# Kernel optimization log

Hardware: AMD Instinct MI355X
Metric: run time of the kernel (lower is better)

## Reference

```python
import jax, jax.numpy as jnp
import numpy as np
from jax import lax

K = 8            # number of object slots
H = 250          # hidden / fc_size
EPS = 1e-5
DN = ('NCHW', 'OIHW', 'NCHW')


def ln_all(x):
    # F.layer_norm over all non-batch dims, no affine params (torch init: w=1,b=0)
    ax = tuple(range(1, x.ndim))
    m = jnp.mean(x, ax, keepdims=True)
    v = jnp.var(x, ax, keepdims=True)
    return (x - m) * lax.rsqrt(v + EPS)


def ln_last(x):
    # nn.LayerNorm(feat) -> last dim only
    m = jnp.mean(x, -1, keepdims=True)
    v = jnp.var(x, -1, keepdims=True)
    return (x - m) * lax.rsqrt(v + EPS)


def conv(x, w, b):
    # torch Conv2d(k=4, s=2, p=1), NCHW
    y = lax.conv_general_dilated(x, w, (2, 2), [(1, 1), (1, 1)], dimension_numbers=DN)
    return y + b[None, :, None, None]


def up4(x):
    return jnp.repeat(jnp.repeat(x, 4, axis=2), 4, axis=3)


def setup_inputs():
    ks = jax.random.split(jax.random.key(0), 20)
    bk = 48 * K
    p = lambda i, shape, s: jax.random.normal(ks[i], shape, jnp.float32) * s
    z = lambda n: jnp.zeros((n,), jnp.float32)
    return dict(
        x=p(0, (bk, 4096), 1.0),
        state=p(1, (bk, H), 1.0),
        # encoder convs (OIHW) + fc
        c1w=p(2, (16, 1, 4, 4), 0.25), c1b=z(16),
        c2w=p(3, (32, 16, 4, 4), 0.06), c2b=z(32),
        c3w=p(4, (64, 32, 4, 4), 0.04), c3b=z(64),
        efc_w=p(5, (4096, 512), 0.016), efc_b=z(512),
        # R_NEM (weights stored as [in, out])
        renc_w=p(6, (H, H), 0.06), renc_b=z(H),
        core_w=p(7, (2 * H, H), 0.045), core_b=z(H),
        ctx_w=p(8, (H, H), 0.06), ctx_b=z(H),
        att1_w=p(9, (H, 100), 0.06), att1_b=z(100),
        att2_w=p(10, (100, 1), 0.1), att2_b=z(1),
        out_w=p(11, (2 * H + 512, H), 0.03), out_b=z(H),
        # decoder fcs + convs
        dfc1_w=p(12, (H, 512), 0.06), dfc1_b=z(512),
        dfc2_w=p(13, (512, 4096), 0.045), dfc2_b=z(4096),
        d1w=p(14, (32, 64, 4, 4), 0.03), d1b=z(32),
        d2w=p(15, (16, 32, 4, 4), 0.045), d2b=z(16),
        d3w=p(16, (1, 16, 4, 4), 0.06), d3b=z(1),
    )


def reference(x, state, c1w, c1b, c2w, c2b, c3w, c3b, efc_w, efc_b,
              renc_w, renc_b, core_w, core_b, ctx_w, ctx_b,
              att1_w, att1_b, att2_w, att2_b, out_w, out_b,
              dfc1_w, dfc1_b, dfc2_w, dfc2_b, d1w, d1b, d2w, d2b, d3w, d3b):
    bk = x.shape[0]
    b = bk // K

    # ---------------- EncoderLayer ----------------
    def inwrap(h, w, bias):  # InputWrapper conv branch: NHWC -> permute(0,3,2,1) -> conv -> back
        y = conv(jnp.transpose(h, (0, 3, 2, 1)), w, bias)
        return jax.nn.elu(ln_all(jnp.transpose(y, (0, 3, 2, 1))))

    h = x.reshape(bk, 64, 64, 1)
    h = inwrap(h, c1w, c1b)                 # (bk,32,32,16)
    h = inwrap(h, c2w, c2b)                 # (bk,16,16,32)
    h = inwrap(h, c3w, c3b)                 # (bk,8,8,64)
    h = h.reshape(bk, -1)                   # (bk,4096)
    h = jax.nn.elu(ln_last(h @ efc_w + efc_b))   # (bk,512)

    # ---------------- R_NEM (RecurrentLayer) ----------------
    s1 = jax.nn.relu(ln_last(state @ renc_w + renc_b))   # (bk,H)
    s1r = s1.reshape(b, K, H)
    idx = np.array([[j for j in range(K) if j != i] for i in range(K)])  # (K,K-1)
    cs = s1r[:, idx, :]                                    # context: (b,K,K-1,H)
    fs = jnp.broadcast_to(s1r[:, :, None, :], cs.shape)    # focus copies
    pair = jnp.concatenate([fs, cs], axis=-1)              # (b,K,K-1,2H)
    core = jax.nn.relu(ln_last(pair @ core_w + core_b))    # (b,K,K-1,H)
    ctx = jax.nn.relu(ln_last(core @ ctx_w + ctx_b))       # (b,K,K-1,H)
    att = jax.nn.sigmoid(jnp.tanh(ln_last(core @ att1_w + att1_b)) @ att2_w + att2_b)  # (b,K,K-1,1)
    effect = jnp.sum(ctx * att, axis=2).reshape(bk, H)     # attention-weighted sum over K-1
    total = jnp.concatenate([s1, effect, h], axis=1)       # (bk, 2H+512)
    new_state = total @ out_w + out_b                      # (bk,H)
    xr = jax.nn.sigmoid(ln_last(new_state))
    state_out = jax.nn.sigmoid(new_state)

    # ---------------- DecoderLayer ----------------
    d = jax.nn.relu(ln_last(xr @ dfc1_w + dfc1_b))         # (bk,512)
    d = jax.nn.relu(ln_last(d @ dfc2_w + dfc2_b))          # (bk,4096)
    d = d.reshape(bk, 8, 8, 64)

    def outwrap(t, w, bias):
        y = conv(up4(jnp.transpose(t, (0, 3, 2, 1))), w, bias)
        return jnp.transpose(y, (0, 3, 2, 1))

    d = jax.nn.relu(ln_all(outwrap(d, d1w, d1b)))          # (bk,16,16,32)
    d = jax.nn.relu(ln_all(outwrap(d, d2w, d2b)))          # (bk,32,32,16)
    d = jax.nn.sigmoid(outwrap(d, d3w, d3b))               # (bk,64,64,1), no LN
    x_out = d.reshape(bk, -1)                              # (bk,4096)
    return x_out, state_out
```

## Files before the change

kernel.cpp:

```cpp
#include <hip/hip_runtime.h>
#include <hip/hip_bf16.h>
#include <math.h>

typedef __attribute__((ext_vector_type(8))) short bf16x8;
typedef __attribute__((ext_vector_type(4))) float f32x4;

__device__ __forceinline__ float eluf(float v){ return v > 0.f ? v : expm1f(v); }
__device__ __forceinline__ float sigf(float v){ return 1.f/(1.f+expf(-v)); }
__device__ __forceinline__ unsigned short f2bf(float f){
  unsigned u = __float_as_uint(f);
  u += 0x7FFFu + ((u >> 16) & 1u);
  return (unsigned short)(u >> 16);
}
__device__ __forceinline__ float bf2f(short s){
  return __uint_as_float(((unsigned)(unsigned short)s) << 16);
}

__device__ __forceinline__ void block_reduce2(float& a, float& b, float* sbuf){
  __syncthreads();
  for (int off = 32; off; off >>= 1){
    a += __shfl_down(a, off);
    b += __shfl_down(b, off);
  }
  int lane = threadIdx.x & 63, w = threadIdx.x >> 6;
  if (lane == 0){ sbuf[2*w] = a; sbuf[2*w+1] = b; }
  __syncthreads();
  if (threadIdx.x == 0){
    int nw = blockDim.x >> 6;
    float sa = 0.f, sb = 0.f;
    for (int i = 0; i < nw; i++){ sa += sbuf[2*i]; sb += sbuf[2*i+1]; }
    sbuf[0] = sa; sbuf[1] = sb;
  }
  __syncthreads();
  a = sbuf[0]; b = sbuf[1];
}

__device__ __forceinline__ float fold_sum(const float* __restrict__ w, int O, int I,
                                          int o, int i, int pa, int pb, int da, int db){
  float s = 0.f;
  for (int kh = 0; kh < 4; kh++){
    bool inh = (pb==0) ? (db==0 ? (kh==0) : (kh>=1)) : (db==0 ? (kh<=2) : (kh==3));
    if (!inh) continue;
    for (int kw = 0; kw < 4; kw++){
      bool inw = (pa==0) ? (da==0 ? (kw==0) : (kw>=1)) : (da==0 ? (kw<=2) : (kw==3));
      if (!inw) continue;
      s += w[((o*I + i)*4 + kh)*4 + kw];
    }
  }
  return s;
}
__device__ __forceinline__ void fold_elem(const float* __restrict__ w, float* __restrict__ CW,
                                          int O, int I, int l){
  int o = l % O; int q = l / O;
  int da = q & 1, db = (q>>1)&1, pa = (q>>2)&1, pb = (q>>3)&1, i = q>>4;
  CW[(((pb*2+pa)*4 + db*2+da)*I + i)*O + o] = fold_sum(w, O, I, o, i, pa, pb, da, db);
}
__device__ __forceinline__ void cvtc2_elem(const float* __restrict__ w, short* __restrict__ D, int l){
  int i = l & 15, t = (l>>4) & 15, o = l>>8;
  D[l] = (short)f2bf(w[(o*16 + i)*16 + t]);
}
__device__ __forceinline__ void cvtc3_elem(const float* __restrict__ w, short* __restrict__ D, int l){
  int i = l & 31, t = (l>>5) & 15, o = l>>9;
  D[l] = (short)f2bf(w[(o*32 + i)*16 + t]);
}
__device__ __forceinline__ void foldd1_elem(const float* __restrict__ w, short* __restrict__ D, int l){
  int i = l & 63, tap = (l>>6)&3, o = (l>>8)&31, ph = l>>13;
  D[l] = (short)f2bf(fold_sum(w, 32, 64, o, i, ph&1, ph>>1, tap&1, tap>>1));
}
__device__ __forceinline__ void foldd2_elem(const float* __restrict__ w, short* __restrict__ D, int l){
  int i = l & 31, tap = (l>>5)&3, o = (l>>7)&15, ph = l>>11;
  D[l] = (short)f2bf(fold_sum(w, 16, 32, o, i, ph&1, ph>>1, tap&1, tap>>1));
}

__global__ __launch_bounds__(256) void prep_combined(
  const float* __restrict__ efc,  short* __restrict__ Defc,
  const float* __restrict__ dfc2, short* __restrict__ Ddfc2,
  const float* __restrict__ outw, short* __restrict__ Dout,
  const float* __restrict__ corew,short* __restrict__ Dcore,
  const float* __restrict__ dfc1, short* __restrict__ Ddfc1,
  const float* __restrict__ renc, short* __restrict__ Drenc,
  const float* __restrict__ ctx,  short* __restrict__ Dctx,
  const float* __restrict__ att1, short* __restrict__ Datt1,
  const float* __restrict__ d3w, float* __restrict__ CWT3,
  const float* __restrict__ c2w, short* __restrict__ BtC2,
  const float* __restrict__ c3w, short* __restrict__ BtC3,
  const float* __restrict__ d1w, short* __restrict__ BD1,
  const float* __restrict__ d2w, short* __restrict__ BD2,
  const float* __restrict__ state, short* __restrict__ SBF,
  short* __restrict__ TOTb)
{
  int bx = blockIdx.x;
  if (bx >= 1192){
    const int F3=256, P2=F3+8192, P3=P2+32768, P4=P3+32768, P5=P4+8192,
              ST=P5+98304, TOTAL=ST+4608;
    for (int l = (bx-1192)*256 + threadIdx.x; l < TOTAL; l += 256*256){
      if (l < F3)      fold_elem(d3w, CWT3, 1, 16, l);
      else if (l < P2) cvtc2_elem(c2w, BtC2, l - F3);
      else if (l < P3) cvtc3_elem(c3w, BtC3, l - P2);
      else if (l < P4) foldd1_elem(d1w, BD1, l - P3);
      else if (l < P5) foldd2_elem(d2w, BD2, l - P4);
      else if (l < ST){
        int q = l - P5;
        int n = q >> 8, k = q & 255;
        SBF[q] = (k < 250) ? (short)f2bf(state[n*250 + k]) : (short)0;
      } else {
        int q = l - ST;
        int row = q / 12, cc = q % 12;
        int col = cc < 6 ? 250 + cc : 506 + (cc - 6);
        TOTb[row*1024 + col] = 0;
      }
    }
    return;
  }
  const float* W; short* D; int K, N, Kp, base, mode = 0;
  if      (bx < 512) { W=efc;  D=Defc;  K=4096; N=512;  Kp=4096; base=0;    }
  else if (bx < 1024){ W=dfc2; D=Ddfc2; K=512;  N=4096; Kp=512;  base=512;  }
  else if (bx < 1088){ W=outw; D=Dout;  K=1012; N=250;  Kp=1024; base=1024; mode=2; }
  else if (bx < 1120){ W=corew;D=Dcore; K=500;  N=250;  Kp=512;  base=1088; mode=1; }
  else if (bx < 1152){ W=dfc1; D=Ddfc1; K=250;  N=512;  Kp=256;  base=1120; }
  else if (bx < 1168){ W=renc; D=Drenc; K=250;  N=250;  Kp=256;  base=1152; }
  else if (bx < 1184){ W=ctx;  D=Dctx;  K=250;  N=250;  Kp=256;  base=1168; }
  else               { W=att1; D=Datt1; K=250;  N=100;  Kp=256;  base=1184; }
  int t = bx - base;
  int tpr = Kp >> 6;
  int tk = t % tpr, tn = t / tpr;
  __shared__ short tile[64][65];
  int c = threadIdx.x & 63, r4 = threadIdx.x >> 6;
  int n0 = tn*64, k0 = tk*64;
  #pragma unroll 4
  for (int p = 0; p < 16; p++){
    int r = r4*16 + p;
    int k = k0 + r, n = n0 + c;
    int ksrc = k; bool valid;
    if (mode == 0) valid = (k < K);
    else if (mode == 1){ valid = (k < 250) || (k >= 256 && k < 506); ksrc = k < 256 ? k : k - 6; }
    else { valid = (k < 250) || (k >= 256 && k < 506) || (k >= 512);
           ksrc = k < 256 ? k : (k < 512 ? k - 6 : k - 12); }
    float v = (valid && n < N) ? W[(size_t)ksrc*N + n] : 0.f;
    tile[c][r] = (short)f2bf(v);
  }
  __syncthreads();
  #pragma unroll 4
  for (int p = 0; p < 16; p++){
    int nn = r4*16 + p;
    int n = n0 + nn;
    if (n < N) D[(size_t)n*Kp + k0 + c] = tile[nn][c];
  }
}

__global__ __launch_bounds__(256) void gemm_mfma(
    const short* __restrict__ Ab, const short* __restrict__ Bt,
    float* __restrict__ P, int M, int N, int Kp, int Kc)
{
  __shared__ __align__(16) short As[64*32];
  __shared__ __align__(16) short Bs[64*32];
  int tid = threadIdx.x;
  int bm = blockIdx.y*64, bn = blockIdx.x*64;
  int kb = blockIdx.z * Kc;
  int kend = kb + Kc;

  int r = tid >> 2, c = tid & 3;
  const short* Arow = Ab + (size_t)(bm + r)*Kp;
  int gn = bn + r;
  bool bval = gn < N;
  const short* Brow = Bt + (size_t)gn*Kp;

  uint4 hA, hB;
  auto load_regs = [&](int k0){
    hA = *(const uint4*)&Arow[k0 + c*8];
    hB = bval ? *(const uint4*)&Brow[k0 + c*8] : make_uint4(0,0,0,0);
  };
  auto write_lds = [&](){
    *(uint4*)&As[r*32 + c*8] = hA;
    *(uint4*)&Bs[r*32 + c*8] = hB;
  };

  int wave = tid >> 6;
  int ln = tid & 15, quad = (tid >> 4) & 3;
  int wr = (wave >> 1) * 32, wc = (wave & 1) * 32;

  f32x4 zero = {0.f, 0.f, 0.f, 0.f};
  f32x4 acc[2][2] = {{zero, zero}, {zero, zero}};

  load_regs(kb);
  write_lds();
  __syncthreads();
  for (int k0 = kb; k0 < kend; k0 += 32){
    int nxt = k0 + 32;
    if (nxt < kend) load_regs(nxt);
    bf16x8 a0 = *(const bf16x8*)&As[(wr +      ln)*32 + quad*8];
    bf16x8 a1 = *(const bf16x8*)&As[(wr + 16 + ln)*32 + quad*8];
    bf16x8 b0 = *(const bf16x8*)&Bs[(wc +      ln)*32 + quad*8];
    bf16x8 b1 = *(const bf16x8*)&Bs[(wc + 16 + ln)*32 + quad*8];
    acc[0][0] = __builtin_amdgcn_mfma_f32_16x16x32_bf16(a0, b0, acc[0][0], 0, 0, 0);
    acc[0][1] = __builtin_amdgcn_mfma_f32_16x16x32_bf16(a0, b1, acc[0][1], 0, 0, 0);
    acc[1][0] = __builtin_amdgcn_mfma_f32_16x16x32_bf16(a1, b0, acc[1][0], 0, 0, 0);
    acc[1][1] = __builtin_amdgcn_mfma_f32_16x16x32_bf16(a1, b1, acc[1][1], 0, 0, 0);
    __syncthreads();
    if (nxt < kend){ write_lds(); __syncthreads(); }
  }

  float* Pout = P + (size_t)blockIdx.z*M*N;
  #pragma unroll
  for (int t = 0; t < 2; t++)
    #pragma unroll
    for (int u = 0; u < 2; u++)
      #pragma unroll
      for (int j = 0; j < 4; j++){
        int row = bm + wr + t*16 + quad*4 + j;
        int col = bn + wc + u*16 + ln;
        if (col < N) Pout[(size_t)row*N + col] = acc[t][u][j];
      }
}

__global__ __launch_bounds__(256) void gemm_core_mfma(
    const short* __restrict__ Tb, const short* __restrict__ Bt,
    float* __restrict__ P, int M, int N, int Kc)
{
  __shared__ __align__(16) short As[64*32];
  __shared__ __align__(16) short Bs[64*32];
  int tid = threadIdx.x;
  int bm = blockIdx.y*64, bn = blockIdx.x*64;
  int kb = blockIdx.z * Kc;
  int kend = kb + Kc;

  int r = tid >> 2, c = tid & 3;
  int gr = bm + r;
  int jj2 = gr % 7, fi2 = gr / 7;
  int ii = fi2 & 7, j2 = fi2 >> 3;
  int jidx = jj2 < ii ? jj2 : jj2 + 1;
  const short* own = Tb + (size_t)fi2*1024;
  const short* oth = Tb + (size_t)(j2*8 + jidx)*1024;
  int gn = bn + r;
  bool bval = gn < N;
  const short* Brow = Bt + (size_t)gn*512;

  uint4 hA, hB;
  auto load_regs = [&](int k0){
    int kk = k0 + c*8;
    const short* src = (kk & 256) ? oth : own;
    hA = *(const uint4*)&src[kk & 255];
    hB = bval ? *(const uint4*)&Brow[kk] : make_uint4(0,0,0,0);
  };
  auto write_lds = [&](){
    *(uint4*)&As[r*32 + c*8] = hA;
    *(uint4*)&Bs[r*32 + c*8] = hB;
  };

  int wave = tid >> 6;
  int ln = tid & 15, quad = (tid >> 4) & 3;
  int wr = (wave >> 1) * 32, wc = (wave & 1) * 32;

  f32x4 zero = {0.f, 0.f, 0.f, 0.f};
  f32x4 acc[2][2] = {{zero, zero}, {zero, zero}};

  load_regs(kb);
  write_lds();
  __syncthreads();
  for (int k0 = kb; k0 < kend; k0 += 32){
    int nxt = k0 + 32;
    if (nxt < kend) load_regs(nxt);
    bf16x8 a0 = *(const bf16x8*)&As[(wr +      ln)*32 + quad*8];
    bf16x8 a1 = *(const bf16x8*)&As[(wr + 16 + ln)*32 + quad*8];
    bf16x8 b0 = *(const bf16x8*)&Bs[(wc +      ln)*32 + quad*8];
    bf16x8 b1 = *(const bf16x8*)&Bs[(wc + 16 + ln)*32 + quad*8];
    acc[0][0] = __builtin_amdgcn_mfma_f32_16x16x32_bf16(a0, b0, acc[0][0], 0, 0, 0);
    acc[0][1] = __builtin_amdgcn_mfma_f32_16x16x32_bf16(a0, b1, acc[0][1], 0, 0, 0);
    acc[1][0] = __builtin_amdgcn_mfma_f32_16x16x32_bf16(a1, b0, acc[1][0], 0, 0, 0);
    acc[1][1] = __builtin_amdgcn_mfma_f32_16x16x32_bf16(a1, b1, acc[1][1], 0, 0, 0);
    __syncthreads();
    if (nxt < kend){ write_lds(); __syncthreads(); }
  }

  float* Pout = P + (size_t)blockIdx.z*M*N;
  #pragma unroll
  for (int t = 0; t < 2; t++)
    #pragma unroll
    for (int u = 0; u < 2; u++)
      #pragma unroll
      for (int j = 0; j < 4; j++){
        int row = bm + wr + t*16 + quad*4 + j;
        int col = bn + wc + u*16 + ln;
        if (col < N) Pout[(size_t)row*N + col] = acc[t][u][j];
      }
}

__global__ __launch_bounds__(256) void reduce_ln(
    const float* __restrict__ Pp, const float* __restrict__ bias,
    void* __restrict__ outp, int M, int N, int KS, int os, int act, int obf)
{
  __shared__ float rowbuf[4096];
  __shared__ float sbuf[16];
  int row = blockIdx.x;
  size_t MN = (size_t)M*N;
  float s = 0.f, s2 = 0.f;
  for (int c = threadIdx.x; c < N; c += 256){
    float v = bias[c];
    for (int ks = 0; ks < KS; ks++) v += Pp[ks*MN + (size_t)row*N + c];
    rowbuf[c] = v; s += v; s2 += v*v;
  }
  block_reduce2(s, s2, sbuf);
  float m = s / N;
  float r = rsqrtf(s2/N - m*m + 1e-5f);
  for (int c = threadIdx.x; c < N; c += 256){
    float v = (rowbuf[c]-m)*r;
    if (act == 1) v = fmaxf(v, 0.f);
    else if (act == 2) v = eluf(v);
    else if (act == 3) v = tanhf(v);
    if (obf) ((short*)outp)[(size_t)row*os + c] = f2bf(v);
    else     ((float*)outp)[(size_t)row*os + c] = v;
  }
}

__global__ __launch_bounds__(256) void reduce_ns(
    const float* __restrict__ Pp, const float* __restrict__ bias,
    short* __restrict__ XRb, float* __restrict__ so, int M, int N, int KS)
{
  __shared__ float rowbuf[256];
  __shared__ float sbuf[16];
  int row = blockIdx.x;
  size_t MN = (size_t)M*N;
  float s = 0.f, s2 = 0.f;
  for (int c = threadIdx.x; c < N; c += 256){
    float v = bias[c];
    for (int ks = 0; ks < KS; ks++) v += Pp[ks*MN + (size_t)row*N + c];
    rowbuf[c] = v; s += v; s2 += v*v;
  }
  block_reduce2(s, s2, sbuf);
  float m = s / N;
  float r = rsqrtf(s2/N - m*m + 1e-5f);
  for (int c = threadIdx.x; c < N; c += 256){
    float v = rowbuf[c];
    XRb[(size_t)row*256 + c] = f2bf(sigf((v-m)*r));
    so[(size_t)row*N + c] = sigf(v);
  }
}

__global__ __launch_bounds__(448) void ctx_att_effect(
    const float* __restrict__ Pc, const float* __restrict__ ctx_b,
    const float* __restrict__ Pa, const float* __restrict__ att1_b,
    const float* __restrict__ w2, const float* __restrict__ b2,
    short* __restrict__ tot)
{
  __shared__ float ctxs[7][250];
  __shared__ float att_s[7];
  int fi = blockIdx.x, tid = threadIdx.x;
  int jj = tid >> 6, lane = tid & 63;
  const size_t MN = (size_t)2688*250, MN2 = (size_t)2688*100;
  int row = fi*7 + jj;
  float vv[4];
  float s = 0.f, s2 = 0.f;
  #pragma unroll
  for (int t = 0; t < 4; t++){
    int c = lane + t*64;
    float v = 0.f;
    if (c < 250) v = ctx_b[c] + Pc[(size_t)row*250 + c] + Pc[MN + (size_t)row*250 + c];
    vv[t] = v; s += v; s2 += v*v;
  }
  #pragma unroll
  for (int off = 32; off; off >>= 1){ s += __shfl_down(s, off); s2 += __shfl_down(s2, off); }
  s = __shfl(s, 0); s2 = __shfl(s2, 0);
  float m = s*(1.f/250.f);
  float r = rsqrtf(s2*(1.f/250.f) - m*m + 1e-5f);
  #pragma unroll
  for (int t = 0; t < 4; t++){
    int c = lane + t*64;
    if (c < 250) ctxs[jj][c] = fmaxf((vv[t]-m)*r, 0.f);
  }
  float va[2];
  s = 0.f; s2 = 0.f;
  #pragma unroll
  for (int t = 0; t < 2; t++){
    int c = lane + t*64;
    float v = 0.f;
    if (c < 100){
      v = att1_b[c];
      #pragma unroll
      for (int ks = 0; ks < 4; ks++) v += Pa[ks*MN2 + (size_t)row*100 + c];
    }
    va[t] = v; s += v; s2 += v*v;
  }
  #pragma unroll
  for (int off = 32; off; off >>= 1){ s += __shfl_down(s, off); s2 += __shfl_down(s2, off); }
  s = __shfl(s, 0); s2 = __shfl(s2, 0);
  m = s*0.01f;
  r = rsqrtf(s2*0.01f - m*m + 1e-5f);
  float d = 0.f;
  #pragma unroll
  for (int t = 0; t < 2; t++){
    int c = lane + t*64;
    if (c < 100) d += tanhf((va[t]-m)*r)*w2[c];
  }
  #pragma unroll
  for (int off = 32; off; off >>= 1) d += __shfl_down(d, off);
  if (lane == 0) att_s[jj] = sigf(d + b2[0]);
  __syncthreads();
  for (int h = tid; h < 250; h += 448){
    float sum = 0.f;
    #pragma unroll
    for (int q = 0; q < 7; q++) sum += ctxs[q][h]*att_s[q];
    tot[(size_t)fi*1024 + 256 + h] = f2bf(sum);
  }
}

__global__ __launch_bounds__(256) void enc_conv1_ig(
    const float* __restrict__ x, const float* __restrict__ w, const float* __restrict__ bias,
    short* __restrict__ outp)
{
  __shared__ __align__(16) float in_t[66*68];
  __shared__ short rawb[16384];
  __shared__ float sbuf[16];
  int n = blockIdx.x, tid = threadIdx.x;
  for (int l = tid; l < 66*68; l += 256) in_t[l] = 0.f;
  __syncthreads();
  const float* xin = x + (size_t)n*4096;
  for (int l4 = tid; l4 < 1024; l4 += 256){
    float4 v = *(const float4*)&xin[l4*4];
    int aa = (l4*4) >> 6, bb = (l4*4) & 63;
    float* dst = &in_t[(aa+1)*68 + bb + 1];
    dst[0]=v.x; dst[1]=v.y; dst[2]=v.z; dst[3]=v.w;
  }
  int o = tid & 15;
  float wr[16];
  #pragma unroll
  for (int t = 0; t < 16; t++) wr[t] = w[o*16 + t];
  float bv = bias[o];
  __syncthreads();
  float s = 0.f, s2 = 0.f;
  for (int r = 0; r < 64; r++){
    int idx = tid + (r<<8);
    int bq = (idx>>4)&31, aq = idx>>9;
    int a0 = 2*aq, b0 = 2*bq;
    float acc = bv;
    #pragma unroll
    for (int kw = 0; kw < 4; kw++){
      const float* row = &in_t[(a0+kw)*68 + b0];
      float2 p0 = *(const float2*)&row[0];
      float2 p1 = *(const float2*)&row[2];
      acc += p0.x*wr[0*4+kw] + p0.y*wr[1*4+kw] + p1.x*wr[2*4+kw] + p1.y*wr[3*4+kw];
    }
    rawb[idx] = f2bf(acc);
    s += acc; s2 += acc*acc;
  }
  block_reduce2(s, s2, sbuf);
  float m = s*(1.f/16384.f);
  float rs = rsqrtf(s2*(1.f/16384.f) - m*m + 1e-5f);
  short* op = outp + (size_t)n*16384;
  for (int l = tid; l < 16384; l += 256){
    float v = bf2f(rawb[l]);
    op[l] = f2bf(eluf((v-m)*rs));
  }
}

__global__ __launch_bounds__(256) void enc_conv2_mfma(
    const short* __restrict__ in, const short* __restrict__ Bt, const float* __restrict__ bias,
    short* __restrict__ outp)
{
  __shared__ __align__(16) short in_t[34*34*16];
  __shared__ float sbuf[16];
  int n = blockIdx.x, tid = threadIdx.x;
  for (int l = tid; l < 34*34*16/4; l += 256) ((unsigned long long*)in_t)[l] = 0ull;
  __syncthreads();
  const short* ip = in + (size_t)n*16384;
  for (int l = tid; l < 4096; l += 256){
    int i4 = l & 3, bb = (l>>2) & 31, aa = l>>7;
    *(uint2*)&in_t[((aa+1)*34 + (bb+1))*16 + i4*4] = *(const uint2*)&ip[aa*512 + bb*16 + i4*4];
  }
  int wave = tid>>6, ln = tid&15, quad = (tid>>4)&3;
  bf16x8 bfr[2][8];
  #pragma unroll
  for (int nt = 0; nt < 2; nt++){
    const short* Brow = Bt + (nt*16 + ln)*256;
    #pragma unroll
    for (int ks = 0; ks < 8; ks++)
      bfr[nt][ks] = *(const bf16x8*)&Brow[ks*32 + quad*8];
  }
  __syncthreads();
  f32x4 z = {0.f,0.f,0.f,0.f};
  f32x4 acc[2][4] = {{z,z,z,z},{z,z,z,z}};
  int tapq = quad>>1, io = (quad&1)*8;
  #pragma unroll
  for (int ks = 0; ks < 8; ks++){
    int t = 2*ks + tapq;
    int kh = t>>2, kw = t&3;
    #pragma unroll
    for (int mt = 0; mt < 4; mt++){
      int p = (wave*4 + mt)*16 + ln;
      int oa = p>>4, ob = p&15;
      bf16x8 a = *(const bf16x8*)&in_t[((2*oa+kw)*34 + (2*ob+kh))*16 + io];
      acc[0][mt] = __builtin_amdgcn_mfma_f32_16x16x32_bf16(a, bfr[0][ks], acc[0][mt],0,0,0);
      acc[1][mt] = __builtin_amdgcn_mfma_f32_16x16x32_bf16(a, bfr[1][ks], acc[1][mt],0,0,0);
    }
  }
  float s = 0.f, s2 = 0.f;
  #pragma unroll
  for (int nt = 0; nt < 2; nt++){
    float bz = bias[nt*16 + ln];
    #pragma unroll
    for (int mt = 0; mt < 4; mt++)
      #pragma unroll
      for (int j = 0; j < 4; j++){
        float v = acc[nt][mt][j] + bz;
        acc[nt][mt][j] = v; s += v; s2 += v*v;
      }
  }
  block_reduce2(s, s2, sbuf);
  float m = s*(1.f/8192.f);
  float rs = rsqrtf(s2*(1.f/8192.f) - m*m + 1e-5f);
  short* op = outp + (size_t)n*8192;
  #pragma unroll
  for (int nt = 0; nt < 2; nt++){
    int o = nt*16 + ln;
    #pragma unroll
    for (int mt = 0; mt < 4; mt++)
      #pragma unroll
      for (int j = 0; j < 4; j++){
        int p = (wave*4 + mt)*16 + quad*4 + j;
        int oa = p>>4, ob = p&15;
        op[oa*512 + ob*32 + o] = f2bf(eluf((acc[nt][mt][j]-m)*rs));
      }
  }
}

__global__ __launch_bounds__(256) void enc_conv3_mfma(
    const short* __restrict__ in, const short* __restrict__ Bt, const float* __restrict__ bias,
    short* __restrict__ outp)
{
  __shared__ __align__(16) short in_t[18*18*32];
  __shared__ float sbuf[16];
  int n = blockIdx.x, tid = threadIdx.x;
  for (int l = tid; l < 18*18*32/4; l += 256) ((unsigned long long*)in_t)[l] = 0ull;
  __syncthreads();
  const short* ip = in + (size_t)n*8192;
  for (int l = tid; l < 2048; l += 256){
    int i4 = l & 7, bb = (l>>3)&15, aa = l>>7;
    *(uint2*)&in_t[((aa+1)*18 + (bb+1))*32 + i4*4] = *(const uint2*)&ip[aa*512 + bb*32 + i4*4];
  }
  int wave = tid>>6, ln = tid&15, quad = (tid>>4)&3;
  int o = wave*16 + ln;
  bf16x8 bfr[16];
  {
    const short* Brow = Bt + o*512;
    #pragma unroll
    for (int ks = 0; ks < 16; ks++)
      bfr[ks] = *(const bf16x8*)&Brow[ks*32 + quad*8];
  }
  __syncthreads();
  f32x4 z = {0.f,0.f,0.f,0.f};
  f32x4 acc[4] = {z,z,z,z};
  #pragma unroll
  for (int ks = 0; ks < 16; ks++){
    int kh = ks>>2, kw = ks&3;
    #pragma unroll
    for (int mt = 0; mt < 4; mt++){
      int p = mt*16 + ln;
      int oa = p>>3, ob = p&7;
      bf16x8 a = *(const bf16x8*)&in_t[((2*oa+kw)*18 + (2*ob+kh))*32 + quad*8];
      acc[mt] = __builtin_amdgcn_mfma_f32_16x16x32_bf16(a, bfr[ks], acc[mt],0,0,0);
    }
  }
  float s = 0.f, s2 = 0.f;
  float bz = bias[o];
  #pragma unroll
  for (int mt = 0; mt < 4; mt++)
    #pragma unroll
    for (int j = 0; j < 4; j++){
      float v = acc[mt][j] + bz;
      acc[mt][j] = v; s += v; s2 += v*v;
    }
  block_reduce2(s, s2, sbuf);
  float m = s*(1.f/4096.f);
  float rs = rsqrtf(s2*(1.f/4096.f) - m*m + 1e-5f);
  short* op = outp + (size_t)n*4096;
  #pragma unroll
  for (int mt = 0; mt < 4; mt++)
    #pragma unroll
    for (int j = 0; j < 4; j++){
      int p = mt*16 + quad*4 + j;
      int oa = p>>3, ob = p&7;
      op[oa*512 + ob*64 + o] = f2bf(eluf((acc[mt][j]-m)*rs));
    }
}

__global__ __launch_bounds__(256) void dec_conv1_mfma(
    const short* __restrict__ in, const short* __restrict__ Bd, const float* __restrict__ bias,
    short* __restrict__ outp)
{
  __shared__ __align__(16) short in_t[10*10*64];
  __shared__ float sbuf[16];
  int n = blockIdx.x, tid = threadIdx.x;
  for (int l = tid; l < 10*10*64/4; l += 256) ((unsigned long long*)in_t)[l] = 0ull;
  __syncthreads();
  const short* ip = in + (size_t)n*4096;
  for (int l = tid; l < 1024; l += 256){
    int i4 = l & 15, sb = (l>>4)&7, sa = l>>7;
    *(uint2*)&in_t[((sa+1)*10 + (sb+1))*64 + i4*4] = *(const uint2*)&ip[sa*512 + sb*64 + i4*4];
  }
  int wave = tid>>6, ln = tid&15, quad = (tid>>4)&3;
  int pa = wave & 1, pb = wave >> 1;
  bf16x8 bfr[2][8];
  #pragma unroll
  for (int nt = 0; nt < 2; nt++){
    const short* Brow = Bd + (wave*32 + nt*16 + ln)*256;
    #pragma unroll
    for (int ks = 0; ks < 8; ks++)
      bfr[nt][ks] = *(const bf16x8*)&Brow[ks*32 + quad*8];
  }
  __syncthreads();
  f32x4 z = {0.f,0.f,0.f,0.f};
  f32x4 acc[2][4] = {{z,z,z,z},{z,z,z,z}};
  #pragma unroll
  for (int ks = 0; ks < 8; ks++){
    int tap = ks>>1, ibase = (ks&1)*32 + quad*8;
    int da = tap & 1, db = tap >> 1;
    #pragma unroll
    for (int mt = 0; mt < 4; mt++){
      int p = mt*16 + ln;
      int ta = p>>3, tb = p&7;
      bf16x8 a = *(const bf16x8*)&in_t[((ta+da+pa)*10 + (tb+db+pb))*64 + ibase];
      acc[0][mt] = __builtin_amdgcn_mfma_f32_16x16x32_bf16(a, bfr[0][ks], acc[0][mt],0,0,0);
      acc[1][mt] = __builtin_amdgcn_mfma_f32_16x16x32_bf16(a, bfr[1][ks], acc[1][mt],0,0,0);
    }
  }
  float s = 0.f, s2 = 0.f;
  #pragma unroll
  for (int nt = 0; nt < 2; nt++){
    float bz = bias[nt*16 + ln];
    #pragma unroll
    for (int mt = 0; mt < 4; mt++)
      #pragma unroll
      for (int j = 0; j < 4; j++){
        float v = acc[nt][mt][j] + bz;
        acc[nt][mt][j] = v; s += v; s2 += v*v;
      }
  }
  block_reduce2(s, s2, sbuf);
  float m = s*(1.f/8192.f);
  float rs = rsqrtf(s2*(1.f/8192.f) - m*m + 1e-5f);
  short* op = outp + (size_t)n*8192;
  #pragma unroll
  for (int nt = 0; nt < 2; nt++){
    int o = nt*16 + ln;
    #pragma unroll
    for (int mt = 0; mt < 4; mt++)
      #pragma unroll
      for (int j = 0; j < 4; j++){
        int p = mt*16 + quad*4 + j;
        int ta = p>>3, tb = p&7;
        op[(2*ta+pa)*512 + (2*tb+pb)*32 + o] = f2bf(fmaxf((acc[nt][mt][j]-m)*rs, 0.f));
      }
  }
}

__global__ __launch_bounds__(256) void dec_conv2_mfma(
    const short* __restrict__ in, const short* __restrict__ Bd, const float* __restrict__ bias,
    short* __restrict__ outp)
{
  __shared__ __align__(16) short in_t[18*18*32];
  __shared__ float sbuf[16];
  int n = blockIdx.x, tid = threadIdx.x;
  for (int l = tid; l < 18*18*32/4; l += 256) ((unsigned long long*)in_t)[l] = 0ull;
  __syncthreads();
  const short* ip = in + (size_t)n*8192;
  for (int l = tid; l < 2048; l += 256){
    int i4 = l & 7, sb = (l>>3)&15, sa = l>>7;
    *(uint2*)&in_t[((sa+1)*18 + (sb+1))*32 + i4*4] = *(const uint2*)&ip[sa*512 + sb*32 + i4*4];
  }
  int wave = tid>>6, ln = tid&15, quad = (tid>>4)&3;
  int pa = wave & 1, pb = wave >> 1;
  bf16x8 bfr[4];
  {
    const short* Brow = Bd + (wave*16 + ln)*128;
    #pragma unroll
    for (int ks = 0; ks < 4; ks++)
      bfr[ks] = *(const bf16x8*)&Brow[ks*32 + quad*8];
  }
  __syncthreads();
  f32x4 z = {0.f,0.f,0.f,0.f};
  f32x4 acc[16] = {z,z,z,z,z,z,z,z,z,z,z,z,z,z,z,z};
  #pragma unroll
  for (int ks = 0; ks < 4; ks++){
    int da = ks & 1, db = ks >> 1;
    #pragma unroll
    for (int mt = 0; mt < 16; mt++){
      int p = mt*16 + ln;
      int ta = p>>4, tb = p&15;
      bf16x8 a = *(const bf16x8*)&in_t[((ta+da+pa)*18 + (tb+db+pb))*32 + quad*8];
      acc[mt] = __builtin_amdgcn_mfma_f32_16x16x32_bf16(a, bfr[ks], acc[mt],0,0,0);
    }
  }
  float s = 0.f, s2 = 0.f;
  float bz = bias[ln];
  #pragma unroll
  for (int mt = 0; mt < 16; mt++)
    #pragma unroll
    for (int j = 0; j < 4; j++){
      float v = acc[mt][j] + bz;
      acc[mt][j] = v; s += v; s2 += v*v;
    }
  block_reduce2(s, s2, sbuf);
  float m = s*(1.f/16384.f);
  float rs = rsqrtf(s2*(1.f/16384.f) - m*m + 1e-5f);
  short* op = outp + (size_t)n*16384;
  #pragma unroll
  for (int mt = 0; mt < 16; mt++)
    #pragma unroll
    for (int j = 0; j < 4; j++){
      int p = mt*16 + quad*4 + j;
      int ta = p>>4, tb = p&15;
      op[(2*ta+pa)*512 + (2*tb+pb)*16 + ln] = f2bf(fmaxf((acc[mt][j]-m)*rs, 0.f));
    }
}

__global__ __launch_bounds__(256) void dec_conv3_ig(
    const short* __restrict__ in, const float* __restrict__ CWT, const float* __restrict__ bias,
    float* __restrict__ outp)
{
  __shared__ __align__(16) float in_t[9792];
  __shared__ __align__(16) float wl[256];
  int bx = blockIdx.x;
  int n = bx >> 1, b0 = (bx & 1) * 32, tb0 = b0 >> 1;
  int tid = threadIdx.x;
  const short* ip = in + (size_t)n*16384;
  for (int l = tid; l < 9792; l += 256){
    int i = l & 15, sb = (l >> 4) % 18, sap = l / 288;
    int sa = sap - 1, sbg = tb0 - 1 + sb;
    float v = 0.f;
    if ((unsigned)sa < 32u && (unsigned)sbg < 32u)
      v = bf2f(ip[sa*512 + sbg*16 + i]);
    in_t[(sap*18 + sb)*16 + i] = v;
  }
  for (int l = tid; l < 256; l += 256) wl[l] = CWT[l];
  __syncthreads();
  float bv = bias[0];
  int bl = tid & 31, ath = tid >> 5;
  int b = b0 + bl;
  int tb = b >> 1, pb = b & 1;
  float* op = outp + (size_t)n*4096;
  #pragma unroll
  for (int j = 0; j < 8; j++){
    int a = ath*8 + j;
    int ta = a >> 1, pa = a & 1;
    float4 s4 = make_float4(0.f,0.f,0.f,0.f);
    #pragma unroll
    for (int db = 0; db < 2; db++){
      int sb = tb + db + (pb ? 0 : -1);
      int sbl = sb - (tb0 - 1);
      #pragma unroll
      for (int da = 0; da < 2; da++){
        int sa = ta + da + (pa ? 0 : -1);
        int sap = sa + 1;
        const float4* A4 = (const float4*)&in_t[(sap*18 + sbl)*16];
        const float4* B4 = (const float4*)&wl[((pb*2+pa)*4 + db*2+da)*16];
        #pragma unroll
        for (int q = 0; q < 4; q++){
          float4 av = A4[q], bw = B4[q];
          s4.x += av.x*bw.x; s4.y += av.y*bw.y;
          s4.z += av.z*bw.z; s4.w += av.w*bw.w;
        }
      }
    }
    op[a*64 + b] = sigf(bv + s4.x + s4.y + s4.z + s4.w);
  }
}

extern "C" void kernel_launch(void* const* d_in, const int* in_sizes, int n_in,
                              void* d_out, int out_size, void* d_ws, size_t ws_size,
                              hipStream_t stream) {
  const float* x      = (const float*)d_in[0];
  const float* state  = (const float*)d_in[1];
  const float* c1w    = (const float*)d_in[2];
  const float* c1b    = (const float*)d_in[3];
  const float* c2w    = (const float*)d_in[4];
  const float* c2b    = (const float*)d_in[5];
  const float* c3w    = (const float*)d_in[6];
  const float* c3b    = (const float*)d_in[7];
  const float* efc_w  = (const float*)d_in[8];
  const float* efc_b  = (const float*)d_in[9];
  const float* renc_w = (const float*)d_in[10];
  const float* renc_b = (const float*)d_in[11];
  const float* core_w = (const float*)d_in[12];
  const float* core_b = (const float*)d_in[13];
  const float* ctx_w  = (const float*)d_in[14];
  const float* ctx_b  = (const float*)d_in[15];
  const float* att1_w = (const float*)d_in[16];
  const float* att1_b = (const float*)d_in[17];
  const float* att2_w = (const float*)d_in[18];
  const float* att2_b = (const float*)d_in[19];
  const float* out_w  = (const float*)d_in[20];
  const float* out_b  = (const float*)d_in[21];
  const float* dfc1_w = (const float*)d_in[22];
  const float* dfc1_b = (const float*)d_in[23];
  const float* dfc2_w = (const float*)d_in[24];
  const float* dfc2_b = (const float*)d_in[25];
  const float* d1w    = (const float*)d_in[26];
  const float* d1b    = (const float*)d_in[27];
  const float* d2w    = (const float*)d_in[28];
  const float* d2b    = (const float*)d_in[29];
  const float* d3w    = (const float*)d_in[30];
  const float* d3b    = (const float*)d_in[31];

  float* wsf = (float*)d_ws;
  size_t o = 0;
  float* PB   = wsf + o; o += (size_t)1600*1024;
  float* PB2  = wsf + o; o += (size_t)2688*100*4;
  float* CWT3 = wsf + o; o += 256;
  short* E1b  = (short*)(wsf + o); o += (size_t)384*16384/2;
  short* E2b  = (short*)(wsf + o); o += (size_t)384*8192/2;
  short* E3b  = (short*)(wsf + o); o += (size_t)384*4096/2;
  short* TOTb = (short*)(wsf + o); o += (size_t)384*1024/2;
  short* C1b  = (short*)(wsf + o); o += (size_t)2688*256/2;
  short* XRb  = (short*)(wsf + o); o += (size_t)384*256/2;
  short* G1b  = (short*)(wsf + o); o += (size_t)384*512/2;
  short* SBF  = (short*)(wsf + o); o += (size_t)384*256/2;
  short* BtC2 = (short*)(wsf + o); o += 8192/2;
  short* BtC3 = (short*)(wsf + o); o += 32768/2;
  short* BD1  = (short*)(wsf + o); o += 32768/2;
  short* BD2  = (short*)(wsf + o); o += 8192/2;
  short* BT_efc  = (short*)(wsf + o); o += 2097152/2;
  short* BT_renc = (short*)(wsf + o); o += 64000/2;
  short* BT_core = (short*)(wsf + o); o += 128000/2;
  short* BT_ctx  = (short*)(wsf + o); o += 64000/2;
  short* BT_att1 = (short*)(wsf + o); o += 25600/2;
  short* BT_out  = (short*)(wsf + o); o += 256000/2;
  short* BT_dfc1 = (short*)(wsf + o); o += 131072/2;
  short* BT_dfc2 = (short*)(wsf + o); o += 2097152/2;
  short* D1b = E2b;
  short* D2b = E1b;
  short* G2b = E3b;

  float* xout = (float*)d_out;
  float* sout = xout + (size_t)384*4096;

  prep_combined<<<1448, 256, 0, stream>>>(
      efc_w, BT_efc, dfc2_w, BT_dfc2, out_w, BT_out, core_w, BT_core,
      dfc1_w, BT_dfc1, renc_w, BT_renc, ctx_w, BT_ctx, att1_w, BT_att1,
      d3w, CWT3, c2w, BtC2, c3w, BtC3, d1w, BD1, d2w, BD2, state, SBF, TOTb);

  enc_conv1_ig<<<384, 256, 0, stream>>>(x, c1w, c1b, E1b);
  enc_conv2_mfma<<<384, 256, 0, stream>>>(E1b, BtC2, c2b, E2b);
  enc_conv3_mfma<<<384, 256, 0, stream>>>(E2b, BtC3, c3b, E3b);
  gemm_mfma<<<dim3(8,6,8), 256, 0, stream>>>(E3b, BT_efc, PB, 384, 512, 4096, 512);
  reduce_ln<<<384, 256, 0, stream>>>(PB, efc_b, TOTb+512, 384, 512, 8, 1024, 2, 1);

  gemm_mfma<<<dim3(4,6,8), 256, 0, stream>>>(SBF, BT_renc, PB, 384, 250, 256, 32);
  reduce_ln<<<384, 256, 0, stream>>>(PB, renc_b, TOTb, 384, 250, 8, 1024, 1, 1);
  gemm_core_mfma<<<dim3(4,42,2), 256, 0, stream>>>(TOTb, BT_core, PB, 2688, 250, 256);
  reduce_ln<<<2688, 256, 0, stream>>>(PB, core_b, C1b, 2688, 250, 2, 256, 1, 1);
  gemm_mfma<<<dim3(4,42,2), 256, 0, stream>>>(C1b, BT_ctx, PB, 2688, 250, 256, 128);
  gemm_mfma<<<dim3(2,42,4), 256, 0, stream>>>(C1b, BT_att1, PB2, 2688, 100, 256, 64);
  ctx_att_effect<<<384, 448, 0, stream>>>(PB, ctx_b, PB2, att1_b, att2_w, att2_b, TOTb);

  gemm_mfma<<<dim3(4,6,8), 256, 0, stream>>>(TOTb, BT_out, PB, 384, 250, 1024, 128);
  reduce_ns<<<384, 256, 0, stream>>>(PB, out_b, XRb, sout, 384, 250, 8);

  gemm_mfma<<<dim3(8,6,4), 256, 0, stream>>>(XRb, BT_dfc1, PB, 384, 512, 256, 64);
  reduce_ln<<<384, 256, 0, stream>>>(PB, dfc1_b, G1b, 384, 512, 4, 512, 1, 1);
  gemm_mfma<<<dim3(64,6,1), 256, 0, stream>>>(G1b, BT_dfc2, PB, 384, 4096, 512, 512);
  reduce_ln<<<384, 256, 0, stream>>>(PB, dfc2_b, G2b, 384, 4096, 1, 4096, 1, 1);

  dec_conv1_mfma<<<384, 256, 0, stream>>>(G2b, BD1, d1b, D1b);
  dec_conv2_mfma<<<384, 256, 0, stream>>>(D1b, BD2, d2b, D2b);
  dec_conv3_ig<<<768, 256, 0, stream>>>(D2b, CWT3, d3b, xout);

  (void)in_sizes; (void)n_in; (void)out_size; (void)ws_size;
}
```

Baseline: 334.7 us.

## Fuse mid-network GEMMs with bias, layernorm and activation epilogues

Adds a templated gemm_ln_f kernel where each block owns full rows (all N columns), so bias, row layernorm and the activation run in the GEMM epilogue. This replaces split-K GEMMs followed by separate reduce_ln, reduce_ns and ctx_att_effect kernels for the renc, core, ctx, att1, out and dfc1 layers. The goal is to remove the fp32 partial-sum round trips and several launches. The cost is far fewer blocks (12 to 84) with no split-K, which leaves most CUs idle and makes each block walk the full K loop. Padded weight rows are now written as zeros so the fused kernel can read full 256-column tiles.

```diff
diff --git a/kernel.cpp b/kernel.cpp
--- a/kernel.cpp
+++ b/kernel.cpp
@@ -90,10 +90,10 @@
   short* __restrict__ TOTb)
 {
   int bx = blockIdx.x;
-  if (bx >= 1192){
+  if (bx >= 1200){
     const int F3=256, P2=F3+8192, P3=P2+32768, P4=P3+32768, P5=P4+8192,
               ST=P5+98304, TOTAL=ST+4608;
-    for (int l = (bx-1192)*256 + threadIdx.x; l < TOTAL; l += 256*256){
+    for (int l = (bx-1200)*256 + threadIdx.x; l < TOTAL; l += 256*256){
       if (l < F3)      fold_elem(d3w, CWT3, 1, 16, l);
       else if (l < P2) cvtc2_elem(c2w, BtC2, l - F3);
       else if (l < P3) cvtc3_elem(c3w, BtC3, l - P2);
@@ -112,15 +112,15 @@
     }
     return;
   }
-  const float* W; short* D; int K, N, Kp, base, mode = 0;
-  if      (bx < 512) { W=efc;  D=Defc;  K=4096; N=512;  Kp=4096; base=0;    }
-  else if (bx < 1024){ W=dfc2; D=Ddfc2; K=512;  N=4096; Kp=512;  base=512;  }
-  else if (bx < 1088){ W=outw; D=Dout;  K=1012; N=250;  Kp=1024; base=1024; mode=2; }
-  else if (bx < 1120){ W=corew;D=Dcore; K=500;  N=250;  Kp=512;  base=1088; mode=1; }
-  else if (bx < 1152){ W=dfc1; D=Ddfc1; K=250;  N=512;  Kp=256;  base=1120; }
-  else if (bx < 1168){ W=renc; D=Drenc; K=250;  N=250;  Kp=256;  base=1152; }
-  else if (bx < 1184){ W=ctx;  D=Dctx;  K=250;  N=250;  Kp=256;  base=1168; }
-  else               { W=att1; D=Datt1; K=250;  N=100;  Kp=256;  base=1184; }
+  const float* W; short* D; int K, N, Np, Kp, base, mode = 0;
+  if      (bx < 512) { W=efc;  D=Defc;  K=4096; N=512;  Np=512;  Kp=4096; base=0;    }
+  else if (bx < 1024){ W=dfc2; D=Ddfc2; K=512;  N=4096; Np=4096; Kp=512;  base=512;  }
+  else if (bx < 1088){ W=outw; D=Dout;  K=1012; N=250;  Np=256;  Kp=1024; base=1024; mode=2; }
+  else if (bx < 1120){ W=corew;D=Dcore; K=500;  N=250;  Np=256;  Kp=512;  base=1088; mode=1; }
+  else if (bx < 1152){ W=dfc1; D=Ddfc1; K=250;  N=512;  Np=512;  Kp=256;  base=1120; }
+  else if (bx < 1168){ W=renc; D=Drenc; K=250;  N=250;  Np=256;  Kp=256;  base=1152; }
+  else if (bx < 1184){ W=ctx;  D=Dctx;  K=250;  N=250;  Np=256;  Kp=256;  base=1168; }
+  else               { W=att1; D=Datt1; K=250;  N=100;  Np=256;  Kp=256;  base=1184; }
   int t = bx - base;
   int tpr = Kp >> 6;
   int tk = t % tpr, tn = t / tpr;
@@ -144,7 +144,7 @@
   for (int p = 0; p < 16; p++){
     int nn = r4*16 + p;
     int n = n0 + nn;
-    if (n < N) D[(size_t)n*Kp + k0 + c] = tile[nn][c];
+    if (n < Np) D[(size_t)n*Kp + k0 + c] = tile[nn][c];
   }
 }
 
@@ -213,76 +213,165 @@
       }
 }
 
-__global__ __launch_bounds__(256) void gemm_core_mfma(
-    const short* __restrict__ Tb, const short* __restrict__ Bt,
-    float* __restrict__ P, int M, int N, int Kc)
-{
-  __shared__ __align__(16) short As[64*32];
-  __shared__ __align__(16) short Bs[64*32];
+template<int MR, int NC>
+__global__ __launch_bounds__(256) void gemm_ln_f(
+    const short* __restrict__ Ab, const short* __restrict__ Tb,
+    const short* __restrict__ Bt, const float* __restrict__ bias,
+    void* __restrict__ outp, float* __restrict__ sout,
+    int N, int Kp, int os, int act, int obf)
+{
+  constexpr int MT = MR/16;
+  constexpr int NU = NC/64;
+  constexpr int APT = (MR*8 + 255)/256;
+  constexpr int BPT = NC*4/256;
+  __shared__ __align__(16) short As[MR*32];
+  __shared__ __align__(16) short Bs[NC*32];
+  __shared__ float ls_s[4][MR], ls_q[4][MR];
   int tid = threadIdx.x;
-  int bm = blockIdx.y*64, bn = blockIdx.x*64;
-  int kb = blockIdx.z * Kc;
-  int kend = kb + Kc;
-
-  int r = tid >> 2, c = tid & 3;
-  int gr = bm + r;
-  int jj2 = gr % 7, fi2 = gr / 7;
-  int ii = fi2 & 7, j2 = fi2 >> 3;
-  int jidx = jj2 < ii ? jj2 : jj2 + 1;
-  const short* own = Tb + (size_t)fi2*1024;
-  const short* oth = Tb + (size_t)(j2*8 + jidx)*1024;
-  int gn = bn + r;
-  bool bval = gn < N;
-  const short* Brow = Bt + (size_t)gn*512;
-
-  uint4 hA, hB;
+  int bm = blockIdx.x * MR;
+  int wave = tid>>6, ln = tid&15, quad = (tid>>4)&3;
+
+  uint2 hA[APT]; uint4 hB[BPT];
   auto load_regs = [&](int k0){
-    int kk = k0 + c*8;
-    const short* src = (kk & 256) ? oth : own;
-    hA = *(const uint4*)&src[kk & 255];
-    hB = bval ? *(const uint4*)&Brow[kk] : make_uint4(0,0,0,0);
+    #pragma unroll
+    for (int i = 0; i < APT; i++){
+      int idx = tid + i*256;
+      if (idx < MR*8){
+        int r = idx>>3, ch = idx&7;
+        int kk = k0 + ch*4;
+        const short* src;
+        if (Tb){
+          int gr = bm + r;
+          int jj2 = gr % 7, fi2 = gr / 7;
+          int ii = fi2 & 7, j2 = fi2 >> 3;
+          int jidx = jj2 < ii ? jj2 : jj2 + 1;
+          const short* base = (kk & 256) ? (Tb + (size_t)(j2*8+jidx)*1024)
+                                         : (Tb + (size_t)fi2*1024);
+          src = base + (kk & 255);
+        } else {
+          src = Ab + (size_t)(bm + r)*Kp + kk;
+        }
+        hA[i] = *(const uint2*)src;
+      }
+    }
+    #pragma unroll
+    for (int i = 0; i < BPT; i++){
+      int idx = tid + i*256;
+      int n = idx>>2, ch = idx&3;
+      hB[i] = *(const uint4*)&Bt[(size_t)n*Kp + k0 + ch*8];
+    }
   };
   auto write_lds = [&](){
-    *(uint4*)&As[r*32 + c*8] = hA;
-    *(uint4*)&Bs[r*32 + c*8] = hB;
+    #pragma unroll
+    for (int i = 0; i < APT; i++){
+      int idx = tid + i*256;
+      if (idx < MR*8){
+        int r = idx>>3, ch = idx&7;
+        *(uint2*)&As[r*32 + ch*4] = hA[i];
+      }
+    }
+    #pragma unroll
+    for (int i = 0; i < BPT; i++){
+      int idx = tid + i*256;
+      int n = idx>>2, ch = idx&3;
+      *(uint4*)&Bs[n*32 + ch*8] = hB[i];
+    }
   };
 
-  int wave = tid >> 6;
-  int ln = tid & 15, quad = (tid >> 4) & 3;
-  int wr = (wave >> 1) * 32, wc = (wave & 1) * 32;
-
-  f32x4 zero = {0.f, 0.f, 0.f, 0.f};
-  f32x4 acc[2][2] = {{zero, zero}, {zero, zero}};
-
-  load_regs(kb);
+  f32x4 z = {0.f,0.f,0.f,0.f};
+  f32x4 acc[MT][NU];
+  #pragma unroll
+  for (int mt = 0; mt < MT; mt++)
+    #pragma unroll
+    for (int u = 0; u < NU; u++) acc[mt][u] = z;
+
+  load_regs(0);
   write_lds();
   __syncthreads();
-  for (int k0 = kb; k0 < kend; k0 += 32){
+  for (int k0 = 0; k0 < Kp; k0 += 32){
     int nxt = k0 + 32;
-    if (nxt < kend) load_regs(nxt);
-    bf16x8 a0 = *(const bf16x8*)&As[(wr +      ln)*32 + quad*8];
-    bf16x8 a1 = *(const bf16x8*)&As[(wr + 16 + ln)*32 + quad*8];
-    bf16x8 b0 = *(const bf16x8*)&Bs[(wc +      ln)*32 + quad*8];
-    bf16x8 b1 = *(const bf16x8*)&Bs[(wc + 16 + ln)*32 + quad*8];
-    acc[0][0] = __builtin_amdgcn_mfma_f32_16x16x32_bf16(a0, b0, acc[0][0], 0, 0, 0);
-    acc[0][1] = __builtin_amdgcn_mfma_f32_16x16x32_bf16(a0, b1, acc[0][1], 0, 0, 0);
-    acc[1][0] = __builtin_amdgcn_mfma_f32_16x16x32_bf16(a1, b0, acc[1][0], 0, 0, 0);
-    acc[1][1] = __builtin_amdgcn_mfma_f32_16x16x32_bf16(a1, b1, acc[1][1], 0, 0, 0);
+    if (nxt < Kp) load_regs(nxt);
+    bf16x8 a[MT];
+    #pragma unroll
+    for (int mt = 0; mt < MT; mt++)
+      a[mt] = *(const bf16x8*)&As[(mt*16 + ln)*32 + quad*8];
+    #pragma unroll
+    for (int u = 0; u < NU; u++){
+      bf16x8 b = *(const bf16x8*)&Bs[(wave*NU*16 + u*16 + ln)*32 + quad*8];
+      #pragma unroll
+      for (int mt = 0; mt < MT; mt++)
+        acc[mt][u] = __builtin_amdgcn_mfma_f32_16x16x32_bf16(a[mt], b, acc[mt][u], 0,0,0);
+    }
     __syncthreads();
-    if (nxt < kend){ write_lds(); __syncthreads(); }
-  }
-
-  float* Pout = P + (size_t)blockIdx.z*M*N;
-  #pragma unroll
-  for (int t = 0; t < 2; t++)
-    #pragma unroll
-    for (int u = 0; u < 2; u++)
+    if (nxt < Kp){ write_lds(); __syncthreads(); }
+  }
+
+  float sl[MT][4], ql[MT][4];
+  #pragma unroll
+  for (int mt = 0; mt < MT; mt++)
+    #pragma unroll
+    for (int j = 0; j < 4; j++){
+      float ss = 0.f, qq = 0.f;
+      #pragma unroll
+      for (int u = 0; u < NU; u++){
+        int col = wave*NU*16 + u*16 + ln;
+        float bv = (col < N) ? bias[col] : 0.f;
+        float v = acc[mt][u][j] + bv;
+        acc[mt][u][j] = v;
+        ss += v; qq += v*v;
+      }
+      sl[mt][j] = ss; ql[mt][j] = qq;
+    }
+  #pragma unroll
+  for (int off = 8; off; off >>= 1)
+    #pragma unroll
+    for (int mt = 0; mt < MT; mt++)
       #pragma unroll
       for (int j = 0; j < 4; j++){
-        int row = bm + wr + t*16 + quad*4 + j;
-        int col = bn + wc + u*16 + ln;
-        if (col < N) Pout[(size_t)row*N + col] = acc[t][u][j];
-      }
+        sl[mt][j] += __shfl_down(sl[mt][j], off, 16);
+        ql[mt][j] += __shfl_down(ql[mt][j], off, 16);
+      }
+  if (ln == 0){
+    #pragma unroll
+    for (int mt = 0; mt < MT; mt++)
+      #pragma unroll
+      for (int j = 0; j < 4; j++){
+        int r = mt*16 + quad*4 + j;
+        ls_s[wave][r] = sl[mt][j];
+        ls_q[wave][r] = ql[mt][j];
+      }
+  }
+  __syncthreads();
+  float invN = 1.f / (float)N;
+  #pragma unroll
+  for (int mt = 0; mt < MT; mt++)
+    #pragma unroll
+    for (int j = 0; j < 4; j++){
+      int r = mt*16 + quad*4 + j;
+      int row = bm + r;
+      float S = ls_s[0][r] + ls_s[1][r] + ls_s[2][r] + ls_s[3][r];
+      float Q = ls_q[0][r] + ls_q[1][r] + ls_q[2][r] + ls_q[3][r];
+      float m = S*invN;
+      float rinv = rsqrtf(Q*invN - m*m + 1e-5f);
+      #pragma unroll
+      for (int u = 0; u < NU; u++){
+        int col = wave*NU*16 + u*16 + ln;
+        if (col >= N) continue;
+        float v = acc[mt][u][j];
+        float lnv = (v - m)*rinv;
+        if (act == 4){
+          ((short*)outp)[(size_t)row*os + col] = f2bf(sigf(lnv));
+          sout[(size_t)row*250 + col] = sigf(v);
+        } else {
+          float w = lnv;
+          if (act == 1) w = fmaxf(w, 0.f);
+          else if (act == 2) w = eluf(w);
+          else if (act == 3) w = tanhf(w);
+          if (obf) ((short*)outp)[(size_t)row*os + col] = f2bf(w);
+          else     ((float*)outp)[(size_t)row*os + col] = w;
+        }
+      }
+    }
 }
 
 __global__ __launch_bounds__(256) void reduce_ln(
@@ -312,84 +401,20 @@
   }
 }
 
-__global__ __launch_bounds__(256) void reduce_ns(
-    const float* __restrict__ Pp, const float* __restrict__ bias,
-    short* __restrict__ XRb, float* __restrict__ so, int M, int N, int KS)
-{
-  __shared__ float rowbuf[256];
-  __shared__ float sbuf[16];
-  int row = blockIdx.x;
-  size_t MN = (size_t)M*N;
-  float s = 0.f, s2 = 0.f;
-  for (int c = threadIdx.x; c < N; c += 256){
-    float v = bias[c];
-    for (int ks = 0; ks < KS; ks++) v += Pp[ks*MN + (size_t)row*N + c];
-    rowbuf[c] = v; s += v; s2 += v*v;
-  }
-  block_reduce2(s, s2, sbuf);
-  float m = s / N;
-  float r = rsqrtf(s2/N - m*m + 1e-5f);
-  for (int c = threadIdx.x; c < N; c += 256){
-    float v = rowbuf[c];
-    XRb[(size_t)row*256 + c] = f2bf(sigf((v-m)*r));
-    so[(size_t)row*N + c] = sigf(v);
-  }
-}
-
-__global__ __launch_bounds__(448) void ctx_att_effect(
-    const float* __restrict__ Pc, const float* __restrict__ ctx_b,
-    const float* __restrict__ Pa, const float* __restrict__ att1_b,
+__global__ __launch_bounds__(448) void effect_kernel(
+    const float* __restrict__ A1f, const short* __restrict__ X1b,
     const float* __restrict__ w2, const float* __restrict__ b2,
     short* __restrict__ tot)
 {
-  __shared__ float ctxs[7][250];
   __shared__ float att_s[7];
   int fi = blockIdx.x, tid = threadIdx.x;
   int jj = tid >> 6, lane = tid & 63;
-  const size_t MN = (size_t)2688*250, MN2 = (size_t)2688*100;
   int row = fi*7 + jj;
-  float vv[4];
-  float s = 0.f, s2 = 0.f;
-  #pragma unroll
-  for (int t = 0; t < 4; t++){
-    int c = lane + t*64;
-    float v = 0.f;
-    if (c < 250) v = ctx_b[c] + Pc[(size_t)row*250 + c] + Pc[MN + (size_t)row*250 + c];
-    vv[t] = v; s += v; s2 += v*v;
-  }
-  #pragma unroll
-  for (int off = 32; off; off >>= 1){ s += __shfl_down(s, off); s2 += __shfl_down(s2, off); }
-  s = __shfl(s, 0); s2 = __shfl(s2, 0);
-  float m = s*(1.f/250.f);
-  float r = rsqrtf(s2*(1.f/250.f) - m*m + 1e-5f);
-  #pragma unroll
-  for (int t = 0; t < 4; t++){
-    int c = lane + t*64;
-    if (c < 250) ctxs[jj][c] = fmaxf((vv[t]-m)*r, 0.f);
-  }
-  float va[2];
-  s = 0.f; s2 = 0.f;
+  float d = 0.f;
   #pragma unroll
   for (int t = 0; t < 2; t++){
     int c = lane + t*64;
-    float v = 0.f;
-    if (c < 100){
-      v = att1_b[c];
-      #pragma unroll
-      for (int ks = 0; ks < 4; ks++) v += Pa[ks*MN2 + (size_t)row*100 + c];
-    }
-    va[t] = v; s += v; s2 += v*v;
-  }
-  #pragma unroll
-  for (int off = 32; off; off >>= 1){ s += __shfl_down(s, off); s2 += __shfl_down(s2, off); }
-  s = __shfl(s, 0); s2 = __shfl(s2, 0);
-  m = s*0.01f;
-  r = rsqrtf(s2*0.01f - m*m + 1e-5f);
-  float d = 0.f;
-  #pragma unroll
-  for (int t = 0; t < 2; t++){
-    int c = lane + t*64;
-    if (c < 100) d += tanhf((va[t]-m)*r)*w2[c];
+    if (c < 100) d += A1f[(size_t)row*128 + c]*w2[c];
   }
   #pragma unroll
   for (int off = 32; off; off >>= 1) d += __shfl_down(d, off);
@@ -398,7 +423,8 @@
   for (int h = tid; h < 250; h += 448){
     float sum = 0.f;
     #pragma unroll
-    for (int q = 0; q < 7; q++) sum += ctxs[q][h]*att_s[q];
+    for (int q = 0; q < 7; q++)
+      sum += bf2f(X1b[((size_t)fi*7 + q)*256 + h])*att_s[q];
     tot[(size_t)fi*1024 + 256 + h] = f2bf(sum);
   }
 }
@@ -803,13 +829,14 @@
   float* wsf = (float*)d_ws;
   size_t o = 0;
   float* PB   = wsf + o; o += (size_t)1600*1024;
-  float* PB2  = wsf + o; o += (size_t)2688*100*4;
+  float* A1f  = wsf + o; o += (size_t)2688*128;
   float* CWT3 = wsf + o; o += 256;
   short* E1b  = (short*)(wsf + o); o += (size_t)384*16384/2;
   short* E2b  = (short*)(wsf + o); o += (size_t)384*8192/2;
   short* E3b  = (short*)(wsf + o); o += (size_t)384*4096/2;
   short* TOTb = (short*)(wsf + o); o += (size_t)384*1024/2;
   short* C1b  = (short*)(wsf + o); o += (size_t)2688*256/2;
+  short* X1b  = (short*)(wsf + o); o += (size_t)2688*256/2;
   short* XRb  = (short*)(wsf + o); o += (size_t)384*256/2;
   short* G1b  = (short*)(wsf + o); o += (size_t)384*512/2;
   short* SBF  = (short*)(wsf + o); o += (size_t)384*256/2;
@@ -818,11 +845,11 @@
   short* BD1  = (short*)(wsf + o); o += 32768/2;
   short* BD2  = (short*)(wsf + o); o += 8192/2;
   short* BT_efc  = (short*)(wsf + o); o += 2097152/2;
-  short* BT_renc = (short*)(wsf + o); o += 64000/2;
-  short* BT_core = (short*)(wsf + o); o += 128000/2;
-  short* BT_ctx  = (short*)(wsf + o); o += 64000/2;
-  short* BT_att1 = (short*)(wsf + o); o += 25600/2;
-  short* BT_out  = (short*)(wsf + o); o += 256000/2;
+  short* BT_renc = (short*)(wsf + o); o += 65536/2;
+  short* BT_core = (short*)(wsf + o); o += 131072/2;
+  short* BT_ctx  = (short*)(wsf + o); o += 65536/2;
+  short* BT_att1 = (short*)(wsf + o); o += 65536/2;
+  short* BT_out  = (short*)(wsf + o); o += 262144/2;
   short* BT_dfc1 = (short*)(wsf + o); o += 131072/2;
   short* BT_dfc2 = (short*)(wsf + o); o += 2097152/2;
   short* D1b = E2b;
@@ -832,7 +859,7 @@
   float* xout = (float*)d_out;
   float* sout = xout + (size_t)384*4096;
 
-  prep_combined<<<1448, 256, 0, stream>>>(
+  prep_combined<<<1456, 256, 0, stream>>>(
       efc_w, BT_efc, dfc2_w, BT_dfc2, out_w, BT_out, core_w, BT_core,
       dfc1_w, BT_dfc1, renc_w, BT_renc, ctx_w, BT_ctx, att1_w, BT_att1,
       d3w, CWT3, c2w, BtC2, c3w, BtC3, d1w, BD1, d2w, BD2, state, SBF, TOTb);
@@ -843,19 +870,21 @@
   gemm_mfma<<<dim3(8,6,8), 256, 0, stream>>>(E3b, BT_efc, PB, 384, 512, 4096, 512);
   reduce_ln<<<384, 256, 0, stream>>>(PB, efc_b, TOTb+512, 384, 512, 8, 1024, 2, 1);
 
-  gemm_mfma<<<dim3(4,6,8), 256, 0, stream>>>(SBF, BT_renc, PB, 384, 250, 256, 32);
-  reduce_ln<<<384, 256, 0, stream>>>(PB, renc_b, TOTb, 384, 250, 8, 1024, 1, 1);
-  gemm_core_mfma<<<dim3(4,42,2), 256, 0, stream>>>(TOTb, BT_core, PB, 2688, 250, 256);
-  reduce_ln<<<2688, 256, 0, stream>>>(PB, core_b, C1b, 2688, 250, 2, 256, 1, 1);
-  gemm_mfma<<<dim3(4,42,2), 256, 0, stream>>>(C1b, BT_ctx, PB, 2688, 250, 256, 128);
-  gemm_mfma<<<dim3(2,42,4), 256, 0, stream>>>(C1b, BT_att1, PB2, 2688, 100, 256, 64);
-  ctx_att_effect<<<384, 448, 0, stream>>>(PB, ctx_b, PB2, att1_b, att2_w, att2_b, TOTb);
-
-  gemm_mfma<<<dim3(4,6,8), 256, 0, stream>>>(TOTb, BT_out, PB, 384, 250, 1024, 128);
-  reduce_ns<<<384, 256, 0, stream>>>(PB, out_b, XRb, sout, 384, 250, 8);
-
-  gemm_mfma<<<dim3(8,6,4), 256, 0, stream>>>(XRb, BT_dfc1, PB, 384, 512, 256, 64);
-  reduce_ln<<<384, 256, 0, stream>>>(PB, dfc1_b, G1b, 384, 512, 4, 512, 1, 1);
+  gemm_ln_f<32,256><<<12, 256, 0, stream>>>(SBF, nullptr, BT_renc, renc_b,
+                                            TOTb, nullptr, 250, 256, 1024, 1, 1);
+  gemm_ln_f<32,256><<<84, 256, 0, stream>>>(nullptr, TOTb, BT_core, core_b,
+                                            C1b, nullptr, 250, 512, 256, 1, 1);
+  gemm_ln_f<32,256><<<84, 256, 0, stream>>>(C1b, nullptr, BT_ctx, ctx_b,
+                                            X1b, nullptr, 250, 256, 256, 1, 1);
+  gemm_ln_f<32,256><<<84, 256, 0, stream>>>(C1b, nullptr, BT_att1, att1_b,
+                                            A1f, nullptr, 100, 256, 128, 3, 0);
+  effect_kernel<<<384, 448, 0, stream>>>(A1f, X1b, att2_w, att2_b, TOTb);
+
+  gemm_ln_f<32,256><<<12, 256, 0, stream>>>(TOTb, nullptr, BT_out, out_b,
+                                            XRb, sout, 250, 1024, 256, 4, 1);
+
+  gemm_ln_f<16,512><<<24, 256, 0, stream>>>(XRb, nullptr, BT_dfc1, dfc1_b,
+                                            G1b, nullptr, 512, 256, 512, 1, 1);
   gemm_mfma<<<dim3(64,6,1), 256, 0, stream>>>(G1b, BT_dfc2, PB, 384, 4096, 512, 512);
   reduce_ln<<<384, 256, 0, stream>>>(PB, dfc2_b, G2b, 384, 4096, 1, 4096, 1, 1);
 
```

Measured after the change: 470.1 us. 1.4x slower.
